# Optimization experiments

Hardware: AMD Instinct MI355X
Metric: run time of the kernel (lower is better)

## Reference

```python
import jax, jax.numpy as jnp
import numpy as np

B = 65536
D_IN = 512
H = 512
EPS = 1e-5


def _layernorm(x, gamma, beta):
    # matches torch ref: unbiased std (ddof=1), eps added to std (not var)
    mean = jnp.mean(x, axis=-1, keepdims=True)
    std = jnp.std(x, axis=-1, ddof=1, keepdims=True)
    return gamma * (x - mean) / (std + EPS) + beta


def setup_inputs() -> dict:
    key = jax.random.key(0)
    ks = jax.random.split(key, 16)
    fan_in = D_IN + H
    s = 1.0 / np.sqrt(fan_in)
    inp = {
        "x": jax.random.normal(ks[0], (B, D_IN), dtype=jnp.float32),
        "prev_h": jax.random.normal(ks[1], (B, H), dtype=jnp.float32),
        "prev_c": jax.random.normal(ks[2], (B, H), dtype=jnp.float32),
        # torch Linear: weight [out, in], bias [out]
        "Wf": jax.random.uniform(ks[3], (H, fan_in), jnp.float32, -s, s),
        "bf": jax.random.uniform(ks[4], (H,), jnp.float32, -s, s),
        "Wi": jax.random.uniform(ks[5], (H, fan_in), jnp.float32, -s, s),
        "bi": jax.random.uniform(ks[6], (H,), jnp.float32, -s, s),
        "Wo": jax.random.uniform(ks[7], (H, fan_in), jnp.float32, -s, s),
        "bo": jax.random.uniform(ks[8], (H,), jnp.float32, -s, s),
        "Wj": jax.random.uniform(ks[9], (H, fan_in), jnp.float32, -s, s),
        "bj": jax.random.uniform(ks[10], (H,), jnp.float32, -s, s),
        "gamma_f": jnp.ones((H,), jnp.float32),
        "beta_f": jnp.zeros((H,), jnp.float32),
        "gamma_i": jnp.ones((H,), jnp.float32),
        "beta_i": jnp.zeros((H,), jnp.float32),
        "gamma_o": jnp.ones((H,), jnp.float32),
        "beta_o": jnp.zeros((H,), jnp.float32),
        "gamma_j": jnp.ones((H,), jnp.float32),
        "beta_j": jnp.zeros((H,), jnp.float32),
        "gamma_c": jnp.ones((H,), jnp.float32),
        "beta_c": jnp.zeros((H,), jnp.float32),
    }
    return inp


def reference(x, prev_h, prev_c, Wf, bf, Wi, bi, Wo, bo, Wj, bj,
              gamma_f, beta_f, gamma_i, beta_i, gamma_o, beta_o,
              gamma_j, beta_j, gamma_c, beta_c):
    combined = jnp.concatenate([x, prev_h], axis=-1)  # [B, D_IN+H]
    ft = jax.nn.sigmoid(_layernorm(combined @ Wf.T + bf, gamma_f, beta_f))
    it = jax.nn.sigmoid(_layernorm(combined @ Wi.T + bi, gamma_i, beta_i))
    ot = jax.nn.sigmoid(_layernorm(combined @ Wo.T + bo, gamma_o, beta_o))
    jt = jnp.tanh(_layernorm(combined @ Wj.T + bj, gamma_j, beta_j))
    c = ft * prev_c + jnp.minimum(1.0 - ft, it) * jt
    c = _layernorm(c, gamma_c, beta_c)
    h = ot * c
    return (h, c)
```

## Files before the change

### kernel.cpp

```cpp
#include <hip/hip_runtime.h>
#include <math.h>

#define B_ROWS 65536
#define D_IN   512
#define HDIM   512
#define FAN    1024
#define NCOL   2048
#define EPS    1e-5f

#define BM 256
#define BN 256
#define BK 64
#define KTILES (FAN / BK)
#define NITER  (KTILES / 2)
#define TILES_PER_BLK 4

typedef unsigned short u16;
using bfrag = __attribute__((ext_vector_type(8))) short;
using facc  = __attribute__((ext_vector_type(4))) float;
using us4   = __attribute__((ext_vector_type(4))) unsigned short;
using us8   = __attribute__((ext_vector_type(8))) unsigned short;

static __device__ __forceinline__ u16 f2b(float f) {
    unsigned u = __builtin_bit_cast(unsigned, f);
    u += 0x7fffu + ((u >> 16) & 1u);
    return (u16)(u >> 16);
}
static __device__ __forceinline__ float b2f(u16 h) {
    unsigned u = ((unsigned)h) << 16;
    return __builtin_bit_cast(float, u);
}
static __device__ __forceinline__ void gload16(const u16* g, u16* l) {
    __builtin_amdgcn_global_load_lds(
        (const __attribute__((address_space(1))) void*)g,
        (__attribute__((address_space(3))) void*)l, 16, 0, 0);
}

__global__ void pack_combined(const float* __restrict__ x, const float* __restrict__ ph,
                              u16* __restrict__ comb)
{
    long i = (long)blockIdx.x * 256 + threadIdx.x;
    if (i >= (long)B_ROWS * D_IN / 4) return;
    long e = i * 4;
    long b = e >> 9;
    int  d = (int)(e & 511);
    float4 xv = *(const float4*)(x + e);
    float4 hv = *(const float4*)(ph + e);
    us4 xb = { f2b(xv.x), f2b(xv.y), f2b(xv.z), f2b(xv.w) };
    us4 hb = { f2b(hv.x), f2b(hv.y), f2b(hv.z), f2b(hv.w) };
    *(us4*)(comb + b * FAN + d)        = xb;
    *(us4*)(comb + b * FAN + D_IN + d) = hb;
}

__global__ void pack_w(const float* __restrict__ Wf, const float* __restrict__ Wi,
                       const float* __restrict__ Wo, const float* __restrict__ Wj,
                       u16* __restrict__ Wall)
{
    long i = (long)blockIdx.x * 256 + threadIdx.x;
    if (i >= (long)NCOL * FAN / 4) return;
    long e = i * 4;
    int  g = (int)(e >> 19);
    long rem = e & 524287L;
    const float* src = (g == 0) ? Wf : (g == 1) ? Wi : (g == 2) ? Wo : Wj;
    float4 v = *(const float4*)(src + rem);
    us4 p = { f2b(v.x), f2b(v.y), f2b(v.z), f2b(v.w) };
    *(us4*)(Wall + e) = p;
}

__global__ __launch_bounds__(512)
void gemm_gates(const u16* __restrict__ A, const u16* __restrict__ W, u16* __restrict__ Cg)
{
    __shared__ u16 lds[2][4][8192];

    const int tid  = threadIdx.x;
    const int lane = tid & 63;
    const int wid  = tid >> 6;
    const int wm   = wid >> 2;
    const int wn   = wid & 3;

    const int nwg = gridDim.x;
    const int swz = (blockIdx.x & 7) * (nwg >> 3) + (blockIdx.x >> 3);
    const long bm  = swz >> 1;
    const int  bn4 = (swz & 1) * TILES_PER_BLK;
    const long arow0 = bm * BM;

    const int sr = tid >> 3;
    const int ss = tid & 7;

    facc acc[8][4];
#pragma unroll
    for (int i = 0; i < 8; ++i)
#pragma unroll
        for (int j = 0; j < 4; ++j) acc[i][j] = facc{0.f, 0.f, 0.f, 0.f};

    auto stageHalf = [&](int buf, int half, int ktg) {
        if (ktg >= TILES_PER_BLK * KTILES) ktg = 0;
        const long k0    = (long)(ktg & (KTILES - 1)) * BK;
        const long bcol0 = ((long)bn4 + (ktg >> 4)) * BN;
#pragma unroll
        for (int i = 0; i < 2; ++i) {
            const int r  = sr + i * 64;
            const int sx = ss ^ (r & 7);
            const u16* src = (half < 2)
                ? (A + (arow0 + half * 128 + r) * (long)FAN + k0 + sx * 8)
                : (W + (bcol0 + (half - 2) * 128 + r) * (long)FAN + k0 + sx * 8);
            gload16(src, &lds[buf][half][i * 4096 + wid * 512]);
        }
    };

    stageHalf(0, 0, 0); stageHalf(0, 1, 0); stageHalf(0, 2, 0); stageHalf(0, 3, 0);
    stageHalf(1, 2, 1); stageHalf(1, 3, 1);
    asm volatile("s_waitcnt vmcnt(4)" ::: "memory");
    __builtin_amdgcn_s_barrier();

    const u16* Ah[2] = { &lds[0][wm][0],            &lds[1][wm][0] };
    const u16* Bh[2] = { &lds[0][2 + (wn >> 1)][0], &lds[1][2 + (wn >> 1)][0] };
    const int lrB0 = (wn & 1) * 64;

#pragma unroll 1
    for (int tile = 0; tile < TILES_PER_BLK; ++tile) {
        const int kb = tile * KTILES;
#pragma unroll 1
        for (int t = 0; t < NITER; ++t) {
            bfrag bq[4][2];
#pragma unroll
            for (int p = 0; p < 8; ++p) {
                const int q  = p & 3;
                const int lt = p >> 2;
                bfrag aq[2][2];
                if (q == 0) {
#pragma unroll
                    for (int nf = 0; nf < 4; ++nf)
#pragma unroll
                        for (int kk = 0; kk < 2; ++kk) {
                            const int lr = lrB0 + nf * 16 + (lane & 15);
                            const int sl = (kk * 4 + (lane >> 4)) ^ (lane & 7);
                            bq[nf][kk] = *(const bfrag*)(Bh[lt] + lr * 64 + sl * 8);
                        }
                }
#pragma unroll
                for (int m2 = 0; m2 < 2; ++m2)
#pragma unroll
                    for (int kk = 0; kk < 2; ++kk) {
                        const int lr = (q * 2 + m2) * 16 + (lane & 15);
                        const int sl = (kk * 4 + (lane >> 4)) ^ (lane & 7);
                        aq[m2][kk] = *(const bfrag*)(Ah[lt] + lr * 64 + sl * 8);
                    }
                if (p == 0)      stageHalf(1, 0, kb + 2 * t + 1);
                else if (p == 1) stageHalf(1, 1, kb + 2 * t + 1);
                else if (p == 2) stageHalf(0, 2, kb + 2 * t + 2);
                else if (p == 3) stageHalf(0, 3, kb + 2 * t + 2);
                else if (p == 4) stageHalf(0, 0, kb + 2 * t + 2);
                else if (p == 5) stageHalf(0, 1, kb + 2 * t + 2);
                else if (p == 6) stageHalf(1, 2, kb + 2 * t + 3);
                else             stageHalf(1, 3, kb + 2 * t + 3);

                if (q == 0) asm volatile("s_waitcnt lgkmcnt(8)" ::: "memory");
                __builtin_amdgcn_s_barrier();
                asm volatile("s_waitcnt lgkmcnt(0)" ::: "memory");
                __builtin_amdgcn_s_setprio(1);
#pragma unroll
                for (int m2 = 0; m2 < 2; ++m2)
#pragma unroll
                    for (int nf = 0; nf < 4; ++nf)
#pragma unroll
                        for (int kk = 0; kk < 2; ++kk)
                            acc[q * 2 + m2][nf] = __builtin_amdgcn_mfma_f32_16x16x32_bf16(
                                aq[m2][kk], bq[nf][kk], acc[q * 2 + m2][nf], 0, 0, 0);
                __builtin_amdgcn_s_setprio(0);
                if (q == 3) asm volatile("s_waitcnt vmcnt(4)" ::: "memory");
                __builtin_amdgcn_s_barrier();
            }
        }

        const long bcol0 = ((long)bn4 + tile) * BN;
#pragma unroll
        for (int mf = 0; mf < 8; ++mf)
#pragma unroll
            for (int nf = 0; nf < 4; ++nf) {
                const long row = arow0 + wm * 128 + mf * 16 + ((lane >> 4) << 2);
                const long col = bcol0 + wn * 64 + nf * 16 + (lane & 15);
                u16* p = Cg + row * (long)NCOL + col;
#pragma unroll
                for (int r = 0; r < 4; ++r) p[(long)r * NCOL] = f2b(acc[mf][nf][r]);
                acc[mf][nf] = facc{0.f, 0.f, 0.f, 0.f};
            }
    }
}

static __device__ __forceinline__ void wave_meanrstd(float s, float ss, float& mean, float& rstd)
{
#pragma unroll
    for (int o = 1; o < 64; o <<= 1) { s += __shfl_xor(s, o); ss += __shfl_xor(ss, o); }
    mean = s * (1.f / 512.f);
    float var = (ss - 512.f * mean * mean) * (1.f / 511.f);
    rstd = 1.f / (sqrtf(fmaxf(var, 0.f)) + EPS);
}
static __device__ __forceinline__ float fast_sigmoid(float z) {
    return __fdividef(1.f, 1.f + __expf(-z));
}
static __device__ __forceinline__ float fast_tanh(float z) {
    return __fdividef(2.f, 1.f + __expf(-2.f * z)) - 1.f;
}

__global__ __launch_bounds__(256)
void lstm_act(const u16* __restrict__ pre, const float* __restrict__ pc,
              const float* __restrict__ bf_, const float* __restrict__ bi_,
              const float* __restrict__ bo_, const float* __restrict__ bj_,
              const float* __restrict__ gf, const float* __restrict__ btf,
              const float* __restrict__ gi, const float* __restrict__ bti,
              const float* __restrict__ go, const float* __restrict__ bto,
              const float* __restrict__ gj, const float* __restrict__ btj,
              const float* __restrict__ gc, const float* __restrict__ btc,
              float* __restrict__ out_h, float* __restrict__ out_c)
{
    const long row  = (long)blockIdx.x * 4 + (threadIdx.x >> 6);
    const int  lane = threadIdx.x & 63;
    const int  c0   = lane * 8;

    const float* bs[4]  = { bf_, bi_, bo_, bj_ };
    const float* gs[4]  = { gf, gi, go, gj };
    const float* bts[4] = { btf, bti, bto, btj };

    float a[4][8];
#pragma unroll
    for (int g = 0; g < 4; ++g) {
        us8 pv = *(const us8*)(pre + row * NCOL + g * HDIM + c0);
        float4 bv0 = *(const float4*)(bs[g] + c0);
        float4 bv1 = *(const float4*)(bs[g] + c0 + 4);
        float bb[8] = { bv0.x, bv0.y, bv0.z, bv0.w, bv1.x, bv1.y, bv1.z, bv1.w };
        float y[8];
        float s = 0.f, ssum = 0.f;
#pragma unroll
        for (int e = 0; e < 8; ++e) {
            y[e] = b2f(pv[e]) + bb[e];
            s += y[e]; ssum += y[e] * y[e];
        }
        float mean, rstd;
        wave_meanrstd(s, ssum, mean, rstd);
        float4 g0 = *(const float4*)(gs[g] + c0);
        float4 g1 = *(const float4*)(gs[g] + c0 + 4);
        float4 t0 = *(const float4*)(bts[g] + c0);
        float4 t1 = *(const float4*)(bts[g] + c0 + 4);
        float gg[8] = { g0.x, g0.y, g0.z, g0.w, g1.x, g1.y, g1.z, g1.w };
        float tt[8] = { t0.x, t0.y, t0.z, t0.w, t1.x, t1.y, t1.z, t1.w };
#pragma unroll
        for (int e = 0; e < 8; ++e) {
            float z = (y[e] - mean) * rstd * gg[e] + tt[e];
            a[g][e] = (g == 3) ? fast_tanh(z) : fast_sigmoid(z);
        }
    }

    float4 p0 = *(const float4*)(pc + row * HDIM + c0);
    float4 p1 = *(const float4*)(pc + row * HDIM + c0 + 4);
    float pcv[8] = { p0.x, p0.y, p0.z, p0.w, p1.x, p1.y, p1.z, p1.w };
    float cr[8];
    float s = 0.f, ssum = 0.f;
#pragma unroll
    for (int e = 0; e < 8; ++e) {
        cr[e] = a[0][e] * pcv[e] + fminf(1.f - a[0][e], a[1][e]) * a[3][e];
        s += cr[e]; ssum += cr[e] * cr[e];
    }
    float mean, rstd;
    wave_meanrstd(s, ssum, mean, rstd);
    float4 gc0 = *(const float4*)(gc + c0);
    float4 gc1 = *(const float4*)(gc + c0 + 4);
    float4 tc0 = *(const float4*)(btc + c0);
    float4 tc1 = *(const float4*)(btc + c0 + 4);
    float gg[8] = { gc0.x, gc0.y, gc0.z, gc0.w, gc1.x, gc1.y, gc1.z, gc1.w };
    float tt[8] = { tc0.x, tc0.y, tc0.z, tc0.w, tc1.x, tc1.y, tc1.z, tc1.w };
    float hv[8], cv[8];
#pragma unroll
    for (int e = 0; e < 8; ++e) {
        float cc = (cr[e] - mean) * rstd * gg[e] + tt[e];
        cv[e] = cc;
        hv[e] = a[2][e] * cc;
    }
    *(float4*)(out_h + row * HDIM + c0)     = make_float4(hv[0], hv[1], hv[2], hv[3]);
    *(float4*)(out_h + row * HDIM + c0 + 4) = make_float4(hv[4], hv[5], hv[6], hv[7]);
    *(float4*)(out_c + row * HDIM + c0)     = make_float4(cv[0], cv[1], cv[2], cv[3]);
    *(float4*)(out_c + row * HDIM + c0 + 4) = make_float4(cv[4], cv[5], cv[6], cv[7]);
}

static __device__ __forceinline__ void ln_pair(
    float y0, float y1,
    const float* __restrict__ gam, const float* __restrict__ bet, int c0,
    float* red, int lane, int wid, float& o0, float& o1)
{
    float s = y0 + y1, ss = y0 * y0 + y1 * y1;
#pragma unroll
    for (int o = 32; o; o >>= 1) { s += __shfl_down(s, o); ss += __shfl_down(ss, o); }
    if (lane == 0) { red[wid * 2] = s; red[wid * 2 + 1] = ss; }
    __syncthreads();
    float S  = red[0] + red[2] + red[4] + red[6];
    float SS = red[1] + red[3] + red[5] + red[7];
    __syncthreads();
    float mean = S * (1.f / 512.f);
    float var  = (SS - 512.f * mean * mean) * (1.f / 511.f);
    float rstd = 1.f / (sqrtf(fmaxf(var, 0.f)) + EPS);
    o0 = (y0 - mean) * rstd * gam[c0]     + bet[c0];
    o1 = (y1 - mean) * rstd * gam[c0 + 1] + bet[c0 + 1];
}

__global__ __launch_bounds__(256)
void lstm_naive(const float* __restrict__ x, const float* __restrict__ ph, const float* __restrict__ pc,
                const float* __restrict__ Wf, const float* __restrict__ bf_,
                const float* __restrict__ Wi, const float* __restrict__ bi_,
                const float* __restrict__ Wo, const float* __restrict__ bo_,
                const float* __restrict__ Wj, const float* __restrict__ bj_,
                const float* __restrict__ gf, const float* __restrict__ btf,
                const float* __restrict__ gi, const float* __restrict__ bti,
                const float* __restrict__ go, const float* __restrict__ bto,
                const float* __restrict__ gj, const float* __restrict__ btj,
                const float* __restrict__ gc, const float* __restrict__ btc,
                float* __restrict__ out_h, float* __restrict__ out_c)
{
    __shared__ float comb[FAN];
    __shared__ float red[8];
    const int b = blockIdx.x, t = threadIdx.x;
    const int lane = t & 63, wid = t >> 6;
    for (int k = t; k < D_IN; k += 256) {
        comb[k]        = x[(long)b * D_IN + k];
        comb[D_IN + k] = ph[(long)b * HDIM + k];
    }
    __syncthreads();
    const int c0 = t * 2;
    const float* Ws[4]  = { Wf, Wi, Wo, Wj };
    const float* bs[4]  = { bf_, bi_, bo_, bj_ };
    const float* gs[4]  = { gf, gi, go, gj };
    const float* bts[4] = { btf, bti, bto, btj };
    float a[4][2];
#pragma unroll
    for (int g = 0; g < 4; ++g) {
        float y[2];
#pragma unroll
        for (int e = 0; e < 2; ++e) {
            const float4* w4 = (const float4*)(Ws[g] + (long)(c0 + e) * FAN);
            const float4* c4 = (const float4*)comb;
            float s = 0.f;
            for (int k = 0; k < FAN / 4; ++k) {
                float4 wv = w4[k], cv = c4[k];
                s += wv.x * cv.x + wv.y * cv.y + wv.z * cv.z + wv.w * cv.w;
            }
            y[e] = s + bs[g][c0 + e];
        }
        ln_pair(y[0], y[1], gs[g], bts[g], c0, red, lane, wid, a[g][0], a[g][1]);
        if (g == 3) { a[g][0] = tanhf(a[g][0]); a[g][1] = tanhf(a[g][1]); }
        else        { a[g][0] = 1.f / (1.f + expf(-a[g][0]));
                      a[g][1] = 1.f / (1.f + expf(-a[g][1])); }
    }
    float2 pcv = *(const float2*)(pc + (long)b * HDIM + c0);
    float f0 = a[0][0], i0 = a[1][0], o0 = a[2][0], j0 = a[3][0];
    float f1 = a[0][1], i1 = a[1][1], o1 = a[2][1], j1 = a[3][1];
    float cr0 = f0 * pcv.x + fminf(1.f - f0, i0) * j0;
    float cr1 = f1 * pcv.y + fminf(1.f - f1, i1) * j1;
    float cc0, cc1;
    ln_pair(cr0, cr1, gc, btc, c0, red, lane, wid, cc0, cc1);
    *(float2*)(out_h + (long)b * HDIM + c0) = make_float2(o0 * cc0, o1 * cc1);
    *(float2*)(out_c + (long)b * HDIM + c0) = make_float2(cc0, cc1);
}

extern "C" void kernel_launch(void* const* d_in, const int* in_sizes, int n_in,
                              void* d_out, int out_size, void* d_ws, size_t ws_size,
                              hipStream_t stream)
{
    const float* x   = (const float*)d_in[0];
    const float* ph  = (const float*)d_in[1];
    const float* pc  = (const float*)d_in[2];
    const float* Wf  = (const float*)d_in[3];
    const float* bf_ = (const float*)d_in[4];
    const float* Wi  = (const float*)d_in[5];
    const float* bi_ = (const float*)d_in[6];
    const float* Wo  = (const float*)d_in[7];
    const float* bo_ = (const float*)d_in[8];
    const float* Wj  = (const float*)d_in[9];
    const float* bj_ = (const float*)d_in[10];
    const float* gf  = (const float*)d_in[11];
    const float* btf = (const float*)d_in[12];
    const float* gi  = (const float*)d_in[13];
    const float* bti = (const float*)d_in[14];
    const float* go  = (const float*)d_in[15];
    const float* bto = (const float*)d_in[16];
    const float* gj  = (const float*)d_in[17];
    const float* btj = (const float*)d_in[18];
    const float* gc  = (const float*)d_in[19];
    const float* btc = (const float*)d_in[20];
    float* out_h = (float*)d_out;
    float* out_c = out_h + (size_t)B_ROWS * HDIM;

    const size_t combElems  = (size_t)B_ROWS * FAN;
    const size_t wElems     = (size_t)NCOL * FAN;
    const size_t fixedBytes = (combElems + wElems) * 2;

    long slabRows = 0;
    if (ws_size > fixedBytes) {
        size_t avail = ws_size - fixedBytes;
        slabRows = (long)(avail / ((size_t)NCOL * 2));
        slabRows &= ~1023L;
        if (slabRows > B_ROWS) slabRows = B_ROWS;
    }

    if (slabRows >= 1024) {
        u16* comb = (u16*)d_ws;
        u16* Wall = comb + combElems;
        u16* pre  = Wall + wElems;
        pack_combined<<<dim3((unsigned)((B_ROWS * (long)D_IN / 4 + 255) / 256)), dim3(256), 0, stream>>>(x, ph, comb);
        pack_w<<<dim3((unsigned)(((long)NCOL * FAN / 4 + 255) / 256)), dim3(256), 0, stream>>>(Wf, Wi, Wo, Wj, Wall);
        for (long r0 = 0; r0 < B_ROWS; r0 += slabRows) {
            long rows = B_ROWS - r0; if (rows > slabRows) rows = slabRows;
            const unsigned nwg = (unsigned)((rows / BM) * 2);
            gemm_gates<<<dim3(nwg), dim3(512), 0, stream>>>(comb + r0 * FAN, Wall, pre);
            lstm_act<<<dim3((unsigned)(rows / 4)), dim3(256), 0, stream>>>(
                pre, pc + r0 * HDIM,
                bf_, bi_, bo_, bj_,
                gf, btf, gi, bti, go, bto, gj, btj, gc, btc,
                out_h + r0 * HDIM, out_c + r0 * HDIM);
        }
    } else {
        lstm_naive<<<dim3(B_ROWS), dim3(256), 0, stream>>>(
            x, ph, pc, Wf, bf_, Wi, bi_, Wo, bo_, Wj, bj_,
            gf, btf, gi, bti, go, bto, gj, btj, gc, btc, out_h, out_c);
    }
}
```

Measured before the change: 526.3 us.

## Fuse gate GEMM with LSTM activation epilogue in one kernel per row block

```diff
diff --git a/kernel.cpp b/kernel.cpp
--- a/kernel.cpp
+++ b/kernel.cpp
@@ -13,7 +13,7 @@
 #define BK 64
 #define KTILES (FAN / BK)
 #define NITER  (KTILES / 2)
-#define TILES_PER_BLK 4
+#define TILES_PER_BLK 8
 
 typedef unsigned short u16;
 using bfrag = __attribute__((ext_vector_type(8))) short;
@@ -34,6 +34,20 @@
     __builtin_amdgcn_global_load_lds(
         (const __attribute__((address_space(1))) void*)g,
         (__attribute__((address_space(3))) void*)l, 16, 0, 0);
+}
+static __device__ __forceinline__ void wave_meanrstd(float s, float ss, float& mean, float& rstd)
+{
+#pragma unroll
+    for (int o = 1; o < 64; o <<= 1) { s += __shfl_xor(s, o); ss += __shfl_xor(ss, o); }
+    mean = s * (1.f / 512.f);
+    float var = (ss - 512.f * mean * mean) * (1.f / 511.f);
+    rstd = 1.f / (sqrtf(fmaxf(var, 0.f)) + EPS);
+}
+static __device__ __forceinline__ float fast_sigmoid(float z) {
+    return __fdividef(1.f, 1.f + __expf(-z));
+}
+static __device__ __forceinline__ float fast_tanh(float z) {
+    return __fdividef(2.f, 1.f + __expf(-2.f * z)) - 1.f;
 }
 
 __global__ void pack_combined(const float* __restrict__ x, const float* __restrict__ ph,
@@ -68,7 +82,16 @@
 }
 
 __global__ __launch_bounds__(512)
-void gemm_gates(const u16* __restrict__ A, const u16* __restrict__ W, u16* __restrict__ Cg)
+void gemm_lstm_fused(const u16* __restrict__ A, const u16* __restrict__ W,
+                     u16* __restrict__ pre, const float* __restrict__ pc,
+                     const float* __restrict__ bf_, const float* __restrict__ bi_,
+                     const float* __restrict__ bo_, const float* __restrict__ bj_,
+                     const float* __restrict__ gf, const float* __restrict__ btf,
+                     const float* __restrict__ gi, const float* __restrict__ bti,
+                     const float* __restrict__ go, const float* __restrict__ bto,
+                     const float* __restrict__ gj, const float* __restrict__ btj,
+                     const float* __restrict__ gc, const float* __restrict__ btc,
+                     float* __restrict__ out_h, float* __restrict__ out_c)
 {
     __shared__ u16 lds[2][4][8192];
 
@@ -80,9 +103,7 @@
 
     const int nwg = gridDim.x;
     const int swz = (blockIdx.x & 7) * (nwg >> 3) + (blockIdx.x >> 3);
-    const long bm  = swz >> 1;
-    const int  bn4 = (swz & 1) * TILES_PER_BLK;
-    const long arow0 = bm * BM;
+    const long arow0 = (long)swz * BM;
 
     const int sr = tid >> 3;
     const int ss = tid & 7;
@@ -96,7 +117,7 @@
     auto stageHalf = [&](int buf, int half, int ktg) {
         if (ktg >= TILES_PER_BLK * KTILES) ktg = 0;
         const long k0    = (long)(ktg & (KTILES - 1)) * BK;
-        const long bcol0 = ((long)bn4 + (ktg >> 4)) * BN;
+        const long bcol0 = (long)(ktg >> 4) * BN;
 #pragma unroll
         for (int i = 0; i < 2; ++i) {
             const int r  = sr + i * 64;
@@ -166,120 +187,98 @@
 #pragma unroll
                         for (int kk = 0; kk < 2; ++kk)
                             acc[q * 2 + m2][nf] = __builtin_amdgcn_mfma_f32_16x16x32_bf16(
-                                aq[m2][kk], bq[nf][kk], acc[q * 2 + m2][nf], 0, 0, 0);
+                                bq[nf][kk], aq[m2][kk], acc[q * 2 + m2][nf], 0, 0, 0);
                 __builtin_amdgcn_s_setprio(0);
                 if (q == 3) asm volatile("s_waitcnt vmcnt(4)" ::: "memory");
                 __builtin_amdgcn_s_barrier();
             }
         }
 
-        const long bcol0 = ((long)bn4 + tile) * BN;
+        const long bcol0 = (long)tile * BN;
 #pragma unroll
         for (int mf = 0; mf < 8; ++mf)
 #pragma unroll
             for (int nf = 0; nf < 4; ++nf) {
-                const long row = arow0 + wm * 128 + mf * 16 + ((lane >> 4) << 2);
-                const long col = bcol0 + wn * 64 + nf * 16 + (lane & 15);
-                u16* p = Cg + row * (long)NCOL + col;
-#pragma unroll
-                for (int r = 0; r < 4; ++r) p[(long)r * NCOL] = f2b(acc[mf][nf][r]);
+                const long m = arow0 + wm * 128 + mf * 16 + (lane & 15);
+                const long n = bcol0 + wn * 64 + nf * 16 + ((lane >> 4) << 2);
+                us4 pk = { f2b(acc[mf][nf][0]), f2b(acc[mf][nf][1]),
+                           f2b(acc[mf][nf][2]), f2b(acc[mf][nf][3]) };
+                *(us4*)(pre + m * (long)NCOL + n) = pk;
                 acc[mf][nf] = facc{0.f, 0.f, 0.f, 0.f};
             }
     }
-}
-
-static __device__ __forceinline__ void wave_meanrstd(float s, float ss, float& mean, float& rstd)
-{
-#pragma unroll
-    for (int o = 1; o < 64; o <<= 1) { s += __shfl_xor(s, o); ss += __shfl_xor(ss, o); }
-    mean = s * (1.f / 512.f);
-    float var = (ss - 512.f * mean * mean) * (1.f / 511.f);
-    rstd = 1.f / (sqrtf(fmaxf(var, 0.f)) + EPS);
-}
-static __device__ __forceinline__ float fast_sigmoid(float z) {
-    return __fdividef(1.f, 1.f + __expf(-z));
-}
-static __device__ __forceinline__ float fast_tanh(float z) {
-    return __fdividef(2.f, 1.f + __expf(-2.f * z)) - 1.f;
-}
-
-__global__ __launch_bounds__(256)
-void lstm_act(const u16* __restrict__ pre, const float* __restrict__ pc,
-              const float* __restrict__ bf_, const float* __restrict__ bi_,
-              const float* __restrict__ bo_, const float* __restrict__ bj_,
-              const float* __restrict__ gf, const float* __restrict__ btf,
-              const float* __restrict__ gi, const float* __restrict__ bti,
-              const float* __restrict__ go, const float* __restrict__ bto,
-              const float* __restrict__ gj, const float* __restrict__ btj,
-              const float* __restrict__ gc, const float* __restrict__ btc,
-              float* __restrict__ out_h, float* __restrict__ out_c)
-{
-    const long row  = (long)blockIdx.x * 4 + (threadIdx.x >> 6);
-    const int  lane = threadIdx.x & 63;
-    const int  c0   = lane * 8;
-
+
+    asm volatile("s_waitcnt vmcnt(0)" ::: "memory");
+    __syncthreads();
+
+    const int c0 = lane * 8;
     const float* bs[4]  = { bf_, bi_, bo_, bj_ };
     const float* gs[4]  = { gf, gi, go, gj };
     const float* bts[4] = { btf, bti, bto, btj };
 
-    float a[4][8];
-#pragma unroll
-    for (int g = 0; g < 4; ++g) {
-        us8 pv = *(const us8*)(pre + row * NCOL + g * HDIM + c0);
-        float4 bv0 = *(const float4*)(bs[g] + c0);
-        float4 bv1 = *(const float4*)(bs[g] + c0 + 4);
-        float bb[8] = { bv0.x, bv0.y, bv0.z, bv0.w, bv1.x, bv1.y, bv1.z, bv1.w };
-        float y[8];
+#pragma unroll 1
+    for (int rr = 0; rr < 32; ++rr) {
+        const long row = arow0 + (long)wid * 32 + rr;
+
+        float a4[4][8];
+#pragma unroll
+        for (int g = 0; g < 4; ++g) {
+            us8 pv = *(const us8*)(pre + row * NCOL + g * HDIM + c0);
+            float4 bv0 = *(const float4*)(bs[g] + c0);
+            float4 bv1 = *(const float4*)(bs[g] + c0 + 4);
+            float bb[8] = { bv0.x, bv0.y, bv0.z, bv0.w, bv1.x, bv1.y, bv1.z, bv1.w };
+            float y[8];
+            float s = 0.f, ssum = 0.f;
+#pragma unroll
+            for (int e = 0; e < 8; ++e) {
+                y[e] = b2f(pv[e]) + bb[e];
+                s += y[e]; ssum += y[e] * y[e];
+            }
+            float mean, rstd;
+            wave_meanrstd(s, ssum, mean, rstd);
+            float4 g0 = *(const float4*)(gs[g] + c0);
+            float4 g1 = *(const float4*)(gs[g] + c0 + 4);
+            float4 t0 = *(const float4*)(bts[g] + c0);
+            float4 t1 = *(const float4*)(bts[g] + c0 + 4);
+            float gg[8] = { g0.x, g0.y, g0.z, g0.w, g1.x, g1.y, g1.z, g1.w };
+            float tt[8] = { t0.x, t0.y, t0.z, t0.w, t1.x, t1.y, t1.z, t1.w };
+#pragma unroll
+            for (int e = 0; e < 8; ++e) {
+                float z = (y[e] - mean) * rstd * gg[e] + tt[e];
+                a4[g][e] = (g == 3) ? fast_tanh(z) : fast_sigmoid(z);
+            }
+        }
+
+        float4 p0 = *(const float4*)(pc + row * HDIM + c0);
+        float4 p1 = *(const float4*)(pc + row * HDIM + c0 + 4);
+        float pcv[8] = { p0.x, p0.y, p0.z, p0.w, p1.x, p1.y, p1.z, p1.w };
+        float cr[8];
         float s = 0.f, ssum = 0.f;
 #pragma unroll
         for (int e = 0; e < 8; ++e) {
-            y[e] = b2f(pv[e]) + bb[e];
-            s += y[e]; ssum += y[e] * y[e];
+            cr[e] = a4[0][e] * pcv[e] + fminf(1.f - a4[0][e], a4[1][e]) * a4[3][e];
+            s += cr[e]; ssum += cr[e] * cr[e];
         }
         float mean, rstd;
         wave_meanrstd(s, ssum, mean, rstd);
-        float4 g0 = *(const float4*)(gs[g] + c0);
-        float4 g1 = *(const float4*)(gs[g] + c0 + 4);
-        float4 t0 = *(const float4*)(bts[g] + c0);
-        float4 t1 = *(const float4*)(bts[g] + c0 + 4);
-        float gg[8] = { g0.x, g0.y, g0.z, g0.w, g1.x, g1.y, g1.z, g1.w };
-        float tt[8] = { t0.x, t0.y, t0.z, t0.w, t1.x, t1.y, t1.z, t1.w };
+        float4 gc0 = *(const float4*)(gc + c0);
+        float4 gc1 = *(const float4*)(gc + c0 + 4);
+        float4 tc0 = *(const float4*)(btc + c0);
+        float4 tc1 = *(const float4*)(btc + c0 + 4);
+        float gg[8] = { gc0.x, gc0.y, gc0.z, gc0.w, gc1.x, gc1.y, gc1.z, gc1.w };
+        float tt[8] = { tc0.x, tc0.y, tc0.z, tc0.w, tc1.x, tc1.y, tc1.z, tc1.w };
+        float hv[8], cv[8];
 #pragma unroll
         for (int e = 0; e < 8; ++e) {
-            float z = (y[e] - mean) * rstd * gg[e] + tt[e];
-            a[g][e] = (g == 3) ? fast_tanh(z) : fast_sigmoid(z);
-        }
-    }
-
-    float4 p0 = *(const float4*)(pc + row * HDIM + c0);
-    float4 p1 = *(const float4*)(pc + row * HDIM + c0 + 4);
-    float pcv[8] = { p0.x, p0.y, p0.z, p0.w, p1.x, p1.y, p1.z, p1.w };
-    float cr[8];
-    float s = 0.f, ssum = 0.f;
-#pragma unroll
-    for (int e = 0; e < 8; ++e) {
-        cr[e] = a[0][e] * pcv[e] + fminf(1.f - a[0][e], a[1][e]) * a[3][e];
-        s += cr[e]; ssum += cr[e] * cr[e];
-    }
-    float mean, rstd;
-    wave_meanrstd(s, ssum, mean, rstd);
-    float4 gc0 = *(const float4*)(gc + c0);
-    float4 gc1 = *(const float4*)(gc + c0 + 4);
-    float4 tc0 = *(const float4*)(btc + c0);
-    float4 tc1 = *(const float4*)(btc + c0 + 4);
-    float gg[8] = { gc0.x, gc0.y, gc0.z, gc0.w, gc1.x, gc1.y, gc1.z, gc1.w };
-    float tt[8] = { tc0.x, tc0.y, tc0.z, tc0.w, tc1.x, tc1.y, tc1.z, tc1.w };
-    float hv[8], cv[8];
-#pragma unroll
-    for (int e = 0; e < 8; ++e) {
-        float cc = (cr[e] - mean) * rstd * gg[e] + tt[e];
-        cv[e] = cc;
-        hv[e] = a[2][e] * cc;
-    }
-    *(float4*)(out_h + row * HDIM + c0)     = make_float4(hv[0], hv[1], hv[2], hv[3]);
-    *(float4*)(out_h + row * HDIM + c0 + 4) = make_float4(hv[4], hv[5], hv[6], hv[7]);
-    *(float4*)(out_c + row * HDIM + c0)     = make_float4(cv[0], cv[1], cv[2], cv[3]);
-    *(float4*)(out_c + row * HDIM + c0 + 4) = make_float4(cv[4], cv[5], cv[6], cv[7]);
+            float cc = (cr[e] - mean) * rstd * gg[e] + tt[e];
+            cv[e] = cc;
+            hv[e] = a4[2][e] * cc;
+        }
+        *(float4*)(out_h + row * HDIM + c0)     = make_float4(hv[0], hv[1], hv[2], hv[3]);
+        *(float4*)(out_h + row * HDIM + c0 + 4) = make_float4(hv[4], hv[5], hv[6], hv[7]);
+        *(float4*)(out_c + row * HDIM + c0)     = make_float4(cv[0], cv[1], cv[2], cv[3]);
+        *(float4*)(out_c + row * HDIM + c0 + 4) = make_float4(cv[4], cv[5], cv[6], cv[7]);
+    }
 }
 
 static __device__ __forceinline__ void ln_pair(
@@ -396,11 +395,11 @@
     if (ws_size > fixedBytes) {
         size_t avail = ws_size - fixedBytes;
         slabRows = (long)(avail / ((size_t)NCOL * 2));
-        slabRows &= ~1023L;
+        slabRows &= ~2047L;
         if (slabRows > B_ROWS) slabRows = B_ROWS;
     }
 
-    if (slabRows >= 1024) {
+    if (slabRows >= 2048) {
         u16* comb = (u16*)d_ws;
         u16* Wall = comb + combElems;
         u16* pre  = Wall + wElems;
@@ -408,10 +407,8 @@
         pack_w<<<dim3((unsigned)(((long)NCOL * FAN / 4 + 255) / 256)), dim3(256), 0, stream>>>(Wf, Wi, Wo, Wj, Wall);
         for (long r0 = 0; r0 < B_ROWS; r0 += slabRows) {
             long rows = B_ROWS - r0; if (rows > slabRows) rows = slabRows;
-            const unsigned nwg = (unsigned)((rows / BM) * 2);
-            gemm_gates<<<dim3(nwg), dim3(512), 0, stream>>>(comb + r0 * FAN, Wall, pre);
-            lstm_act<<<dim3((unsigned)(rows / 4)), dim3(256), 0, stream>>>(
-                pre, pc + r0 * HDIM,
+            gemm_lstm_fused<<<dim3((unsigned)(rows / BM)), dim3(512), 0, stream>>>(
+                comb + r0 * FAN, Wall, pre, pc + r0 * HDIM,
                 bf_, bi_, bo_, bj_,
                 gf, btf, gi, bti, go, bto, gj, btj, gc, btc,
                 out_h + r0 * HDIM, out_c + r0 * HDIM);
```

Result: no change. 518.0 us (-1.6%).

## Fuse bias into GEMM epilogue with transposed MFMA for vector stores, persistent LSTM act

Applied to the files above, without the earlier changes.

```diff
diff --git a/kernel.cpp b/kernel.cpp
--- a/kernel.cpp
+++ b/kernel.cpp
@@ -34,6 +34,20 @@
     __builtin_amdgcn_global_load_lds(
         (const __attribute__((address_space(1))) void*)g,
         (__attribute__((address_space(3))) void*)l, 16, 0, 0);
+}
+static __device__ __forceinline__ void wave_meanrstd(float s, float ss, float& mean, float& rstd)
+{
+#pragma unroll
+    for (int o = 1; o < 64; o <<= 1) { s += __shfl_xor(s, o); ss += __shfl_xor(ss, o); }
+    mean = s * (1.f / 512.f);
+    float var = (ss - 512.f * mean * mean) * (1.f / 511.f);
+    rstd = 1.f / (sqrtf(fmaxf(var, 0.f)) + EPS);
+}
+static __device__ __forceinline__ float fast_sigmoid(float z) {
+    return __fdividef(1.f, 1.f + __expf(-z));
+}
+static __device__ __forceinline__ float fast_tanh(float z) {
+    return __fdividef(2.f, 1.f + __expf(-2.f * z)) - 1.f;
 }
 
 __global__ void pack_combined(const float* __restrict__ x, const float* __restrict__ ph,
@@ -67,8 +81,20 @@
     *(us4*)(Wall + e) = p;
 }
 
+__global__ void pack_bias(const float* __restrict__ bf_, const float* __restrict__ bi_,
+                          const float* __restrict__ bo_, const float* __restrict__ bj_,
+                          float* __restrict__ biasAll)
+{
+    int idx = blockIdx.x * 256 + threadIdx.x;
+    if (idx >= NCOL) return;
+    int g = idx >> 9;
+    const float* s = (g == 0) ? bf_ : (g == 1) ? bi_ : (g == 2) ? bo_ : bj_;
+    biasAll[idx] = s[idx & 511];
+}
+
 __global__ __launch_bounds__(512)
-void gemm_gates(const u16* __restrict__ A, const u16* __restrict__ W, u16* __restrict__ Cg)
+void gemm_gates(const u16* __restrict__ A, const u16* __restrict__ W,
+                const float* __restrict__ biasAll, u16* __restrict__ Cg)
 {
     __shared__ u16 lds[2][4][8192];
 
@@ -166,7 +192,7 @@
 #pragma unroll
                         for (int kk = 0; kk < 2; ++kk)
                             acc[q * 2 + m2][nf] = __builtin_amdgcn_mfma_f32_16x16x32_bf16(
-                                aq[m2][kk], bq[nf][kk], acc[q * 2 + m2][nf], 0, 0, 0);
+                                bq[nf][kk], aq[m2][kk], acc[q * 2 + m2][nf], 0, 0, 0);
                 __builtin_amdgcn_s_setprio(0);
                 if (q == 3) asm volatile("s_waitcnt vmcnt(4)" ::: "memory");
                 __builtin_amdgcn_s_barrier();
@@ -175,111 +201,96 @@
 
         const long bcol0 = ((long)bn4 + tile) * BN;
 #pragma unroll
-        for (int mf = 0; mf < 8; ++mf)
-#pragma unroll
-            for (int nf = 0; nf < 4; ++nf) {
-                const long row = arow0 + wm * 128 + mf * 16 + ((lane >> 4) << 2);
-                const long col = bcol0 + wn * 64 + nf * 16 + (lane & 15);
-                u16* p = Cg + row * (long)NCOL + col;
-#pragma unroll
-                for (int r = 0; r < 4; ++r) p[(long)r * NCOL] = f2b(acc[mf][nf][r]);
+        for (int nf = 0; nf < 4; ++nf) {
+            const long n = bcol0 + wn * 64 + nf * 16 + ((lane >> 4) << 2);
+            float4 bv = *(const float4*)(biasAll + n);
+#pragma unroll
+            for (int mf = 0; mf < 8; ++mf) {
+                const long m = arow0 + wm * 128 + mf * 16 + (lane & 15);
+                us4 pk = { f2b(acc[mf][nf][0] + bv.x), f2b(acc[mf][nf][1] + bv.y),
+                           f2b(acc[mf][nf][2] + bv.z), f2b(acc[mf][nf][3] + bv.w) };
+                *(us4*)(Cg + m * (long)NCOL + n) = pk;
                 acc[mf][nf] = facc{0.f, 0.f, 0.f, 0.f};
             }
-    }
-}
-
-static __device__ __forceinline__ void wave_meanrstd(float s, float ss, float& mean, float& rstd)
-{
-#pragma unroll
-    for (int o = 1; o < 64; o <<= 1) { s += __shfl_xor(s, o); ss += __shfl_xor(ss, o); }
-    mean = s * (1.f / 512.f);
-    float var = (ss - 512.f * mean * mean) * (1.f / 511.f);
-    rstd = 1.f / (sqrtf(fmaxf(var, 0.f)) + EPS);
-}
-static __device__ __forceinline__ float fast_sigmoid(float z) {
-    return __fdividef(1.f, 1.f + __expf(-z));
-}
-static __device__ __forceinline__ float fast_tanh(float z) {
-    return __fdividef(2.f, 1.f + __expf(-2.f * z)) - 1.f;
+        }
+    }
 }
 
 __global__ __launch_bounds__(256)
 void lstm_act(const u16* __restrict__ pre, const float* __restrict__ pc,
-              const float* __restrict__ bf_, const float* __restrict__ bi_,
-              const float* __restrict__ bo_, const float* __restrict__ bj_,
               const float* __restrict__ gf, const float* __restrict__ btf,
               const float* __restrict__ gi, const float* __restrict__ bti,
               const float* __restrict__ go, const float* __restrict__ bto,
               const float* __restrict__ gj, const float* __restrict__ btj,
               const float* __restrict__ gc, const float* __restrict__ btc,
-              float* __restrict__ out_h, float* __restrict__ out_c)
-{
-    const long row  = (long)blockIdx.x * 4 + (threadIdx.x >> 6);
+              float* __restrict__ out_h, float* __restrict__ out_c, long rows)
+{
     const int  lane = threadIdx.x & 63;
     const int  c0   = lane * 8;
-
-    const float* bs[4]  = { bf_, bi_, bo_, bj_ };
+    const long wave = (long)blockIdx.x * 4 + (threadIdx.x >> 6);
+    const long totW = (long)gridDim.x * 4;
+
     const float* gs[4]  = { gf, gi, go, gj };
     const float* bts[4] = { btf, bti, bto, btj };
-
-    float a[4][8];
+    float gg[4][8], tt[4][8], gcv[8], tcv[8];
 #pragma unroll
     for (int g = 0; g < 4; ++g) {
-        us8 pv = *(const us8*)(pre + row * NCOL + g * HDIM + c0);
-        float4 bv0 = *(const float4*)(bs[g] + c0);
-        float4 bv1 = *(const float4*)(bs[g] + c0 + 4);
-        float bb[8] = { bv0.x, bv0.y, bv0.z, bv0.w, bv1.x, bv1.y, bv1.z, bv1.w };
-        float y[8];
+        *(float4*)&gg[g][0] = *(const float4*)(gs[g] + c0);
+        *(float4*)&gg[g][4] = *(const float4*)(gs[g] + c0 + 4);
+        *(float4*)&tt[g][0] = *(const float4*)(bts[g] + c0);
+        *(float4*)&tt[g][4] = *(const float4*)(bts[g] + c0 + 4);
+    }
+    *(float4*)&gcv[0] = *(const float4*)(gc + c0);
+    *(float4*)&gcv[4] = *(const float4*)(gc + c0 + 4);
+    *(float4*)&tcv[0] = *(const float4*)(btc + c0);
+    *(float4*)&tcv[4] = *(const float4*)(btc + c0 + 4);
+
+#pragma unroll 1
+    for (long row = wave; row < rows; row += totW) {
+        float a4[4][8];
+#pragma unroll
+        for (int g = 0; g < 4; ++g) {
+            us8 pv = *(const us8*)(pre + row * NCOL + g * HDIM + c0);
+            float y[8];
+            float s = 0.f, ssum = 0.f;
+#pragma unroll
+            for (int e = 0; e < 8; ++e) {
+                y[e] = b2f(pv[e]);
+                s += y[e]; ssum += y[e] * y[e];
+            }
+            float mean, rstd;
+            wave_meanrstd(s, ssum, mean, rstd);
+#pragma unroll
+            for (int e = 0; e < 8; ++e) {
+                float z = (y[e] - mean) * rstd * gg[g][e] + tt[g][e];
+                a4[g][e] = (g == 3) ? fast_tanh(z) : fast_sigmoid(z);
+            }
+        }
+
+        float4 p0 = *(const float4*)(pc + row * HDIM + c0);
+        float4 p1 = *(const float4*)(pc + row * HDIM + c0 + 4);
+        float pcv[8] = { p0.x, p0.y, p0.z, p0.w, p1.x, p1.y, p1.z, p1.w };
+        float cr[8];
         float s = 0.f, ssum = 0.f;
 #pragma unroll
         for (int e = 0; e < 8; ++e) {
-            y[e] = b2f(pv[e]) + bb[e];
-            s += y[e]; ssum += y[e] * y[e];
+            cr[e] = a4[0][e] * pcv[e] + fminf(1.f - a4[0][e], a4[1][e]) * a4[3][e];
+            s += cr[e]; ssum += cr[e] * cr[e];
         }
         float mean, rstd;
         wave_meanrstd(s, ssum, mean, rstd);
-        float4 g0 = *(const float4*)(gs[g] + c0);
-        float4 g1 = *(const float4*)(gs[g] + c0 + 4);
-        float4 t0 = *(const float4*)(bts[g] + c0);
-        float4 t1 = *(const float4*)(bts[g] + c0 + 4);
-        float gg[8] = { g0.x, g0.y, g0.z, g0.w, g1.x, g1.y, g1.z, g1.w };
-        float tt[8] = { t0.x, t0.y, t0.z, t0.w, t1.x, t1.y, t1.z, t1.w };
+        float hv[8], cv[8];
 #pragma unroll
         for (int e = 0; e < 8; ++e) {
-            float z = (y[e] - mean) * rstd * gg[e] + tt[e];
-            a[g][e] = (g == 3) ? fast_tanh(z) : fast_sigmoid(z);
-        }
-    }
-
-    float4 p0 = *(const float4*)(pc + row * HDIM + c0);
-    float4 p1 = *(const float4*)(pc + row * HDIM + c0 + 4);
-    float pcv[8] = { p0.x, p0.y, p0.z, p0.w, p1.x, p1.y, p1.z, p1.w };
-    float cr[8];
-    float s = 0.f, ssum = 0.f;
-#pragma unroll
-    for (int e = 0; e < 8; ++e) {
-        cr[e] = a[0][e] * pcv[e] + fminf(1.f - a[0][e], a[1][e]) * a[3][e];
-        s += cr[e]; ssum += cr[e] * cr[e];
-    }
-    float mean, rstd;
-    wave_meanrstd(s, ssum, mean, rstd);
-    float4 gc0 = *(const float4*)(gc + c0);
-    float4 gc1 = *(const float4*)(gc + c0 + 4);
-    float4 tc0 = *(const float4*)(btc + c0);
-    float4 tc1 = *(const float4*)(btc + c0 + 4);
-    float gg[8] = { gc0.x, gc0.y, gc0.z, gc0.w, gc1.x, gc1.y, gc1.z, gc1.w };
-    float tt[8] = { tc0.x, tc0.y, tc0.z, tc0.w, tc1.x, tc1.y, tc1.z, tc1.w };
-    float hv[8], cv[8];
-#pragma unroll
-    for (int e = 0; e < 8; ++e) {
-        float cc = (cr[e] - mean) * rstd * gg[e] + tt[e];
-        cv[e] = cc;
-        hv[e] = a[2][e] * cc;
-    }
-    *(float4*)(out_h + row * HDIM + c0)     = make_float4(hv[0], hv[1], hv[2], hv[3]);
-    *(float4*)(out_h + row * HDIM + c0 + 4) = make_float4(hv[4], hv[5], hv[6], hv[7]);
-    *(float4*)(out_c + row * HDIM + c0)     = make_float4(cv[0], cv[1], cv[2], cv[3]);
-    *(float4*)(out_c + row * HDIM + c0 + 4) = make_float4(cv[4], cv[5], cv[6], cv[7]);
+            float cc = (cr[e] - mean) * rstd * gcv[e] + tcv[e];
+            cv[e] = cc;
+            hv[e] = a4[2][e] * cc;
+        }
+        *(float4*)(out_h + row * HDIM + c0)     = make_float4(hv[0], hv[1], hv[2], hv[3]);
+        *(float4*)(out_h + row * HDIM + c0 + 4) = make_float4(hv[4], hv[5], hv[6], hv[7]);
+        *(float4*)(out_c + row * HDIM + c0)     = make_float4(cv[0], cv[1], cv[2], cv[3]);
+        *(float4*)(out_c + row * HDIM + c0 + 4) = make_float4(cv[4], cv[5], cv[6], cv[7]);
+    }
 }
 
 static __device__ __forceinline__ void ln_pair(
@@ -390,7 +401,8 @@
 
     const size_t combElems  = (size_t)B_ROWS * FAN;
     const size_t wElems     = (size_t)NCOL * FAN;
-    const size_t fixedBytes = (combElems + wElems) * 2;
+    const size_t biasBytes  = (size_t)NCOL * sizeof(float);
+    const size_t fixedBytes = (combElems + wElems) * 2 + biasBytes;
 
     long slabRows = 0;
     if (ws_size > fixedBytes) {
@@ -401,20 +413,21 @@
     }
 
     if (slabRows >= 1024) {
-        u16* comb = (u16*)d_ws;
-        u16* Wall = comb + combElems;
-        u16* pre  = Wall + wElems;
+        u16*   comb    = (u16*)d_ws;
+        u16*   Wall    = comb + combElems;
+        float* biasAll = (float*)(Wall + wElems);
+        u16*   pre     = (u16*)(biasAll + NCOL);
         pack_combined<<<dim3((unsigned)((B_ROWS * (long)D_IN / 4 + 255) / 256)), dim3(256), 0, stream>>>(x, ph, comb);
         pack_w<<<dim3((unsigned)(((long)NCOL * FAN / 4 + 255) / 256)), dim3(256), 0, stream>>>(Wf, Wi, Wo, Wj, Wall);
+        pack_bias<<<dim3(8), dim3(256), 0, stream>>>(bf_, bi_, bo_, bj_, biasAll);
         for (long r0 = 0; r0 < B_ROWS; r0 += slabRows) {
             long rows = B_ROWS - r0; if (rows > slabRows) rows = slabRows;
             const unsigned nwg = (unsigned)((rows / BM) * 2);
-            gemm_gates<<<dim3(nwg), dim3(512), 0, stream>>>(comb + r0 * FAN, Wall, pre);
-            lstm_act<<<dim3((unsigned)(rows / 4)), dim3(256), 0, stream>>>(
+            gemm_gates<<<dim3(nwg), dim3(512), 0, stream>>>(comb + r0 * FAN, Wall, biasAll, pre);
+            lstm_act<<<dim3(1024), dim3(256), 0, stream>>>(
                 pre, pc + r0 * HDIM,
-                bf_, bi_, bo_, bj_,
                 gf, btf, gi, bti, go, bto, gj, btj, gc, btc,
-                out_h + r0 * HDIM, out_c + r0 * HDIM);
+                out_h + r0 * HDIM, out_c + r0 * HDIM, rows);
         }
     } else {
         lstm_naive<<<dim3(B_ROWS), dim3(256), 0, stream>>>(
```

After: 561.5 us. +6.7%, slower.
